# Kernel optimization log

Measured on AMD Instinct MI355X. Metric: run time of the kernel, lower is better.

The kernel has to match this reference:

```python
import jax, jax.numpy as jnp
import numpy as np

B, T, I, H, O, TGT = 64, 512, 64, 512, 64, 96
SCALE = 0.05


def setup_inputs() -> dict:
    key = jax.random.key(0)
    ks = jax.random.split(key, 12)
    rn = lambda k, sh: jax.random.normal(k, sh, jnp.float32) * SCALE
    return {
        "x": jax.random.normal(ks[0], (B, T, I), jnp.float32),
        "W_ih0": rn(ks[1], (4 * H, I)),
        "W_hh0": rn(ks[2], (4 * H, H)),
        "b_ih0": rn(ks[3], (4 * H,)),
        "b_hh0": rn(ks[4], (4 * H,)),
        "W_ih1": rn(ks[5], (4 * H, H)),
        "W_hh1": rn(ks[6], (4 * H, H)),
        "b_ih1": rn(ks[7], (4 * H,)),
        "b_hh1": rn(ks[8], (4 * H,)),
        "W_fc": rn(ks[9], (O, H)),
        "b_fc": rn(ks[10], (O,)),
        "target_len": TGT,
    }


def _cell(x_t, h, c, Wi, Wh, b):
    # PyTorch LSTM gate order: i, f, g, o
    g = x_t @ Wi.T + h @ Wh.T + b  # [B, 4H]
    i, f, gg, o = jnp.split(g, 4, axis=-1)
    c_new = jax.nn.sigmoid(f) * c + jax.nn.sigmoid(i) * jnp.tanh(gg)
    h_new = jax.nn.sigmoid(o) * jnp.tanh(c_new)
    return h_new, c_new


def _run_layer(seq_tbf, Wi, Wh, b):
    # seq_tbf: [T, B, F]; returns hidden sequence [T, B, H] and final (h, c)
    nb = seq_tbf.shape[1]
    hdim = Wh.shape[1]
    init = (jnp.zeros((nb, hdim), seq_tbf.dtype), jnp.zeros((nb, hdim), seq_tbf.dtype))

    def step(carry, x_t):
        h, c = _cell(x_t, carry[0], carry[1], Wi, Wh, b)
        return (h, c), h

    (h, c), hs = jax.lax.scan(step, init, seq_tbf)
    return hs, h, c


def reference(x, W_ih0, W_hh0, b_ih0, b_hh0, W_ih1, W_hh1, b_ih1, b_hh1, W_fc, b_fc, target_len):
    # Dropout is inactive (eval-mode reference).
    b0 = b_ih0 + b_hh0
    b1 = b_ih1 + b_hh1

    # --- encoder pass over full context ---
    seq = jnp.transpose(x, (1, 0, 2))                 # [T, B, I]
    hs0, h0, c0 = _run_layer(seq, W_ih0, W_hh0, b0)   # layer 0
    _, h1, c1 = _run_layer(hs0, W_ih1, W_hh1, b1)     # layer 1

    x_in = x[:, -1, :]  # [B, I]

    def dec_step(carry, _):
        h0, c0, h1, c1, xi = carry
        h0, c0 = _cell(xi, h0, c0, W_ih0, W_hh0, b0)
        h1, c1 = _cell(h0, h1, c1, W_ih1, W_hh1, b1)
        y = h1 @ W_fc.T + b_fc  # [B, O], fed back as next input
        return (h0, c0, h1, c1, y), y

    _, ys = jax.lax.scan(dec_step, (h0, c0, h1, c1, x_in), None, length=target_len)
    return jnp.transpose(ys, (1, 0, 2))  # [B, target_len, O]
```

## Files before the change

### kernel.cpp

```cpp
#include <hip/hip_runtime.h>
#include <stdint.h>


#define NWG 256
#define NTH 256

constexpr int Tt = 512, TGT = 96;

typedef __attribute__((ext_vector_type(8))) short bf16x8;
typedef __attribute__((ext_vector_type(4))) float f32x4;
typedef unsigned long long u64;

__device__ __forceinline__ unsigned short f2bf(float f) {
  union { float f; unsigned u; } v; v.f = f;
  return (unsigned short)((v.u + 0x7fffu + ((v.u >> 16) & 1u)) >> 16);
}
__device__ __forceinline__ float bf2f(unsigned short h) {
  union { unsigned u; float f; } v; v.u = ((unsigned)h) << 16; return v.f;
}
__device__ __forceinline__ float sigm(float x) { return 1.f / (1.f + __expf(-x)); }
__device__ __forceinline__ float tanh_(float x) { return 1.f - 2.f / (__expf(2.f * x) + 1.f); }

__device__ __forceinline__ unsigned ald32a(const unsigned* p) {
  return __hip_atomic_load(p, __ATOMIC_RELAXED, __HIP_MEMORY_SCOPE_AGENT);
}
__device__ __forceinline__ void ast32a(unsigned* p, unsigned v) {
  __hip_atomic_store(p, v, __ATOMIC_RELAXED, __HIP_MEMORY_SCOPE_AGENT);
}
__device__ __forceinline__ u64 ald64a(const u64* p) {
  return __hip_atomic_load(p, __ATOMIC_RELAXED, __HIP_MEMORY_SCOPE_AGENT);
}
__device__ __forceinline__ void ast64a(u64* p, u64 v) {
  __hip_atomic_store(p, v, __ATOMIC_RELAXED, __HIP_MEMORY_SCOPE_AGENT);
}

struct SMem {
  unsigned short wB[2][4][16][64][8];
  u64 a0[16 * 68];
  u64 a1[16 * 68];
  unsigned short wfc2[1024];
  float gpart[4][272];
  float fcp[256];
  float b0s[64], b1s[64], b0d[64], bfc2[2];
};

__device__ __forceinline__ int amap(int idx) {
  int b = idx >> 7, k8 = idx & 127;
  return (k8 >> 3) * 68 + b * 8 + (k8 & 7);
}

__device__ __forceinline__ void stage1(u64* dst, const u64* src, int tid) {
  u64 v0 = ald64a(src + tid),       v1 = ald64a(src + tid + 256);
  u64 v2 = ald64a(src + tid + 512), v3 = ald64a(src + tid + 768);
  dst[amap(tid)] = v0; dst[amap(tid + 256)] = v1;
  dst[amap(tid + 512)] = v2; dst[amap(tid + 768)] = v3;
}
__device__ __forceinline__ void stage2(u64* d0, const u64* s0, u64* d1, const u64* s1, int tid) {
  u64 v0 = ald64a(s0 + tid),       v1 = ald64a(s0 + tid + 256);
  u64 v2 = ald64a(s0 + tid + 512), v3 = ald64a(s0 + tid + 768);
  u64 v4 = ald64a(s1 + tid),       v5 = ald64a(s1 + tid + 256);
  u64 v6 = ald64a(s1 + tid + 512), v7 = ald64a(s1 + tid + 768);
  d0[amap(tid)] = v0; d0[amap(tid + 256)] = v1;
  d0[amap(tid + 512)] = v2; d0[amap(tid + 768)] = v3;
  d1[amap(tid)] = v4; d1[amap(tid + 256)] = v5;
  d1[amap(tid + 512)] = v6; d1[amap(tid + 768)] = v7;
}

__device__ __forceinline__ void gbar(unsigned* slots, int g, int w, unsigned tgt) {
  __syncthreads();
  if (threadIdx.x == 0) ast32a(slots + g * 32 + w, tgt);
  if (threadIdx.x < 64) {
    const unsigned* sp = slots + g * 32 + (threadIdx.x & 31);
    while (true) {
      unsigned v = ald32a(sp);
      if (__all((int)(v >= tgt))) break;
      __builtin_amdgcn_s_sleep(1);
    }
  }
  __syncthreads();
}

#define MFMA(a, b, c) __builtin_amdgcn_mfma_f32_16x16x32_bf16(a, b, c, 0, 0, 0)

__global__ __launch_bounds__(NTH, 1) void lstm_kernel(
    const float* __restrict__ x,
    const float* __restrict__ Wih0, const float* __restrict__ Whh0,
    const float* __restrict__ bih0, const float* __restrict__ bhh0,
    const float* __restrict__ Wih1, const float* __restrict__ Whh1,
    const float* __restrict__ bih1, const float* __restrict__ bhh1,
    const float* __restrict__ Wfc, const float* __restrict__ bfc,
    u64* h0q, u64* h1q, unsigned* slots, float* __restrict__ out)
{
  __shared__ SMem sm;
  const int g = blockIdx.x & 7;
  const int wgw = blockIdx.x >> 3;
  const int tid = threadIdx.x;

  for (int e = tid; e < 8192; e += NTH) {
    int m = e >> 12, w4 = (e >> 10) & 3, kc = (e >> 6) & 15, l = e & 63;
    int colx = l & 15, qx = l >> 4;
    size_t row = (size_t)((colx & 3) * 512 + wgw * 16 + w4 * 4 + (colx >> 2));
    const float* src = (m ? Wih1 : Whh0) + row * 512 + kc * 32 + qx * 8;
    unsigned short* dst = &sm.wB[m][w4][kc][l][0];
    float4 u = *(const float4*)src, v = *(const float4*)(src + 4);
    dst[0] = f2bf(u.x); dst[1] = f2bf(u.y); dst[2] = f2bf(u.z); dst[3] = f2bf(u.w);
    dst[4] = f2bf(v.x); dst[5] = f2bf(v.y); dst[6] = f2bf(v.z); dst[7] = f2bf(v.w);
  }
  for (int e = tid; e < 1024; e += NTH)
    sm.wfc2[e] = f2bf(Wfc[(size_t)(wgw * 2 + (e >> 9)) * 512 + (e & 511)]);
  if (tid < 64) {
    int jj = tid >> 2, g4 = tid & 3;
    int grow = g4 * 512 + wgw * 16 + jj;
    float s0 = bih0[grow] + bhh0[grow];
    sm.b0s[tid] = s0;
    sm.b1s[tid] = bih1[grow] + bhh1[grow];
    float ex = 0.f;
    for (int i = 0; i < 64; ++i) ex += Wih0[(size_t)grow * 64 + i] * bfc[i];
    sm.b0d[tid] = s0 + ex;
  }
  if (tid < 2) sm.bfc2[tid] = bfc[wgw * 2 + tid];

  const int wave = tid >> 6, lane = tid & 63;
  const int col = lane & 15, quad = lane >> 4;
  const int koff = quad * 8;
  const size_t rowg = (size_t)((col & 3) * 512 + wgw * 16 + wave * 4 + (col >> 2));

  bf16x8 whh1f[16];
#pragma unroll
  for (int kc = 0; kc < 16; ++kc) {
    const float* p = Whh1 + rowg * 512 + kc * 32 + koff;
    float4 u = *(const float4*)p, v = *(const float4*)(p + 4);
    bf16x8 r;
    r[0] = (short)f2bf(u.x); r[1] = (short)f2bf(u.y); r[2] = (short)f2bf(u.z); r[3] = (short)f2bf(u.w);
    r[4] = (short)f2bf(v.x); r[5] = (short)f2bf(v.y); r[6] = (short)f2bf(v.z); r[7] = (short)f2bf(v.w);
    whh1f[kc] = r;
  }
  bf16x8 wih0f[2];
#pragma unroll
  for (int kc = 0; kc < 2; ++kc) {
    const float* p = Wih0 + rowg * 64 + kc * 32 + koff;
    float4 u = *(const float4*)p, v = *(const float4*)(p + 4);
    bf16x8 r;
    r[0] = (short)f2bf(u.x); r[1] = (short)f2bf(u.y); r[2] = (short)f2bf(u.z); r[3] = (short)f2bf(u.w);
    r[4] = (short)f2bf(v.x); r[5] = (short)f2bf(v.y); r[6] = (short)f2bf(v.z); r[7] = (short)f2bf(v.w);
    wih0f[kc] = r;
  }
  bf16x8 wcombf[16];
  {
    float wc[16][8];
#pragma unroll
    for (int kc = 0; kc < 16; ++kc)
#pragma unroll
      for (int j = 0; j < 8; ++j) wc[kc][j] = 0.f;
    for (int i = 0; i < 64; ++i) {
      float wi = Wih0[rowg * 64 + i];
      const float* fr = Wfc + (size_t)i * 512 + koff;
#pragma unroll
      for (int kc = 0; kc < 16; ++kc) {
        float4 u = *(const float4*)(fr + kc * 32);
        float4 v = *(const float4*)(fr + kc * 32 + 4);
        wc[kc][0] += wi * u.x; wc[kc][1] += wi * u.y;
        wc[kc][2] += wi * u.z; wc[kc][3] += wi * u.w;
        wc[kc][4] += wi * v.x; wc[kc][5] += wi * v.y;
        wc[kc][6] += wi * v.z; wc[kc][7] += wi * v.w;
      }
    }
#pragma unroll
    for (int kc = 0; kc < 16; ++kc) {
      bf16x8 r;
#pragma unroll
      for (int j = 0; j < 8; ++j) r[j] = (short)f2bf(wc[kc][j]);
      wcombf[kc] = r;
    }
  }
  __syncthreads();

  const float b0c = sm.b0s[wave * 16 + col];
  const float b1c = sm.b1s[wave * 16 + col];
  const float b0dc = sm.b0d[wave * 16 + col];
  const unsigned short* pw0 = &sm.wB[0][wave][0][lane][0];
  const unsigned short* pw1 = &sm.wB[1][wave][0][lane][0];
  const u64* afrag0 = sm.a0 + (col & 7) * 8 + quad * 2;
  const u64* afrag1 = sm.a1 + (col & 7) * 8 + quad * 2;
  unsigned ph = 0;
  float c0 = 0.f, c1 = 0.f;
  const size_t xstride = (size_t)Tt * 64;

  auto loadx = [&](const float* p) -> bf16x8 {
    float4 u = *(const float4*)p, v = *(const float4*)(p + 4);
    bf16x8 r;
    r[0] = (short)f2bf(u.x); r[1] = (short)f2bf(u.y); r[2] = (short)f2bf(u.z); r[3] = (short)f2bf(u.w);
    r[4] = (short)f2bf(v.x); r[5] = (short)f2bf(v.y); r[6] = (short)f2bf(v.z); r[7] = (short)f2bf(v.w);
    return r;
  };

  auto actstore = [&](f32x4 v, float& cst, u64* hdst) {
    float* gp = sm.gpart[wave];
#pragma unroll
    for (int r = 0; r < 4; ++r) gp[(quad * 4 + r) * 17 + col] = v[r];
    unsigned hbits = 0;
    int b = lane >> 2, j = lane & 3;
    if (lane < 32) {
      const float* ro = gp + b * 17 + j * 4;
      float iv = sigm(ro[0]), fv = sigm(ro[1]), gv = tanh_(ro[2]), ov = sigm(ro[3]);
      float c = fv * cst + iv * gv; cst = c;
      hbits = f2bf(ov * tanh_(c));
    }
    unsigned h1b = __shfl(hbits, (lane + 1) & 63);
    unsigned h2b = __shfl(hbits, (lane + 2) & 63);
    unsigned h3b = __shfl(hbits, (lane + 3) & 63);
    if (lane < 32 && j == 0) {
      u64 pk = (u64)hbits | ((u64)h1b << 16) | ((u64)h2b << 32) | ((u64)h3b << 48);
      ast64a(hdst + b * 128 + wgw * 4 + wave, pk);
    }
  };

  auto fcpart = [&](const u64* asrc) {
    int ks = tid >> 4, b = (tid >> 1) & 7, cc = tid & 1;
    const unsigned short* hr = (const unsigned short*)(asrc + ks * 68 + b * 8);
    const unsigned short* wp = sm.wfc2 + cc * 512 + ks * 32;
    float s = 0.f;
#pragma unroll
    for (int k2 = 0; k2 < 4; ++k2) {
      bf16x8 hv = *(const bf16x8*)(hr + k2 * 8);
      bf16x8 wv = *(const bf16x8*)(wp + k2 * 8);
#pragma unroll
      for (int q2 = 0; q2 < 8; ++q2) s += bf2f((unsigned short)hv[q2]) * bf2f((unsigned short)wv[q2]);
    }
    sm.fcp[tid] = s;
  };
  auto fcout = [&](int d) {
    if (tid < 16) {
      float sv = sm.bfc2[tid & 1];
#pragma unroll
      for (int k = 0; k < 16; ++k) sv += sm.fcp[k * 16 + tid];
      int bb = tid >> 1, cc = tid & 1;
      out[(size_t)(g * 8 + bb) * (TGT * 64) + d * 64 + (wgw * 2 + cc)] = sv;
    }
  };

  for (int t = 0; t <= Tt; ++t) {
    const u64* h0prev = h0q + ((t + 1) & 1) * 8192 + g * 1024;
    u64* h0cur = h0q + (t & 1) * 8192 + g * 1024;
    const u64* h1prev = h1q + (t & 1) * 8192 + g * 1024;
    u64* h1cur = h1q + ((t + 1) & 1) * 8192 + g * 1024;

    bf16x8 xa0, xa1;
    if (t < Tt) {
      const float* xb = x + (size_t)(g * 8 + (col & 7)) * xstride + (size_t)t * 64 + koff;
      xa0 = loadx(xb); xa1 = loadx(xb + 32);
    }
    if (t == 1)      { stage1(sm.a0, h0prev, tid); __syncthreads(); }
    else if (t >= 2) { stage2(sm.a0, h0prev, sm.a1, h1prev, tid); __syncthreads(); }

    if (t < Tt) {
      f32x4 za = {b0c, b0c, b0c, b0c}, zb = {0.f, 0.f, 0.f, 0.f};
      za = MFMA(xa0, wih0f[0], za);
      zb = MFMA(xa1, wih0f[1], zb);
      if (t >= 1) {
        f32x4 ya = {b1c, b1c, b1c, b1c}, yb = {0.f, 0.f, 0.f, 0.f};
#pragma unroll
        for (int kc = 0; kc < 16; ++kc) {
          bf16x8 a = *(const bf16x8*)(afrag0 + kc * 68);
          bf16x8 w0 = *(const bf16x8*)(pw0 + kc * 512);
          bf16x8 w1 = *(const bf16x8*)(pw1 + kc * 512);
          if (kc & 1) { zb = MFMA(a, w0, zb); yb = MFMA(a, w1, yb); }
          else        { za = MFMA(a, w0, za); ya = MFMA(a, w1, ya); }
        }
        if (t >= 2) {
#pragma unroll
          for (int kc = 0; kc < 16; ++kc) {
            bf16x8 a = *(const bf16x8*)(afrag1 + kc * 68);
            if (kc & 1) yb = MFMA(a, whh1f[kc], yb);
            else        ya = MFMA(a, whh1f[kc], ya);
          }
        }
        actstore(za + zb, c0, h0cur);
        actstore(ya + yb, c1, h1cur);
      } else {
        actstore(za + zb, c0, h0cur);
      }
    } else {
      f32x4 ya = {b1c, b1c, b1c, b1c}, yb = {0.f, 0.f, 0.f, 0.f};
#pragma unroll
      for (int kc = 0; kc < 16; ++kc) {
        bf16x8 a = *(const bf16x8*)(afrag0 + kc * 68);
        bf16x8 w1 = *(const bf16x8*)(pw1 + kc * 512);
        if (kc & 1) yb = MFMA(a, w1, yb);
        else        ya = MFMA(a, w1, ya);
      }
#pragma unroll
      for (int kc = 0; kc < 16; ++kc) {
        bf16x8 a = *(const bf16x8*)(afrag1 + kc * 68);
        if (kc & 1) yb = MFMA(a, whh1f[kc], yb);
        else        ya = MFMA(a, whh1f[kc], ya);
      }
      actstore(ya + yb, c1, h1cur);
    }
    gbar(slots, g, wgw, ++ph);
  }

  {
    stage2(sm.a0, h0q + 8192 + g * 1024, sm.a1, h1q + 8192 + g * 1024, tid);
    __syncthreads();
    const float* xb = x + (size_t)(g * 8 + (col & 7)) * xstride + (size_t)(Tt - 1) * 64 + koff;
    bf16x8 xa0 = loadx(xb), xa1 = loadx(xb + 32);
    f32x4 za = {b0c, b0c, b0c, b0c}, zb = {0.f, 0.f, 0.f, 0.f};
    za = MFMA(xa0, wih0f[0], za);
    zb = MFMA(xa1, wih0f[1], zb);
#pragma unroll
    for (int kc = 0; kc < 16; ++kc) {
      bf16x8 a = *(const bf16x8*)(afrag0 + kc * 68);
      bf16x8 w0 = *(const bf16x8*)(pw0 + kc * 512);
      if (kc & 1) zb = MFMA(a, w0, zb);
      else        za = MFMA(a, w0, za);
    }
    actstore(za + zb, c0, h0q + g * 1024);
  }
  gbar(slots, g, wgw, ++ph);
  {
    stage1(sm.a0, h0q + g * 1024, tid);
    __syncthreads();
    f32x4 ya = {b1c, b1c, b1c, b1c}, yb = {0.f, 0.f, 0.f, 0.f};
#pragma unroll
    for (int kc = 0; kc < 16; ++kc) {
      bf16x8 a = *(const bf16x8*)(afrag0 + kc * 68);
      bf16x8 w1 = *(const bf16x8*)(pw1 + kc * 512);
      bf16x8 a2 = *(const bf16x8*)(afrag1 + kc * 68);
      if (kc & 1) { yb = MFMA(a, w1, yb); yb = MFMA(a2, whh1f[kc], yb); }
      else        { ya = MFMA(a, w1, ya); ya = MFMA(a2, whh1f[kc], ya); }
    }
    actstore(ya + yb, c1, h1q + g * 1024);
  }
  gbar(slots, g, wgw, ++ph);

  for (int d = 1; d < TGT; ++d) {
    {
      stage2(sm.a0, h0q + ((d + 1) & 1) * 8192 + g * 1024,
             sm.a1, h1q + ((d + 1) & 1) * 8192 + g * 1024, tid);
      __syncthreads();
      fcpart(sm.a1);
      f32x4 za = {b0dc, b0dc, b0dc, b0dc}, zb = {0.f, 0.f, 0.f, 0.f};
#pragma unroll
      for (int kc = 0; kc < 16; ++kc) {
        bf16x8 a = *(const bf16x8*)(afrag0 + kc * 68);
        bf16x8 w0 = *(const bf16x8*)(pw0 + kc * 512);
        bf16x8 a2 = *(const bf16x8*)(afrag1 + kc * 68);
        if (kc & 1) { zb = MFMA(a, w0, zb); zb = MFMA(a2, wcombf[kc], zb); }
        else        { za = MFMA(a, w0, za); za = MFMA(a2, wcombf[kc], za); }
      }
      actstore(za + zb, c0, h0q + (d & 1) * 8192 + g * 1024);
      __syncthreads();
      fcout(d - 1);
    }
    gbar(slots, g, wgw, ++ph);

    {
      stage1(sm.a0, h0q + (d & 1) * 8192 + g * 1024, tid);
      __syncthreads();
      f32x4 ya = {b1c, b1c, b1c, b1c}, yb = {0.f, 0.f, 0.f, 0.f};
#pragma unroll
      for (int kc = 0; kc < 16; ++kc) {
        bf16x8 a = *(const bf16x8*)(afrag0 + kc * 68);
        bf16x8 w1 = *(const bf16x8*)(pw1 + kc * 512);
        bf16x8 a2 = *(const bf16x8*)(afrag1 + kc * 68);
        if (kc & 1) { yb = MFMA(a, w1, yb); yb = MFMA(a2, whh1f[kc], yb); }
        else        { ya = MFMA(a, w1, ya); ya = MFMA(a2, whh1f[kc], ya); }
      }
      actstore(ya + yb, c1, h1q + (d & 1) * 8192 + g * 1024);
    }
    gbar(slots, g, wgw, ++ph);
  }

  {
    stage1(sm.a1, h1q + 8192 + g * 1024, tid);
    __syncthreads();
    fcpart(sm.a1);
    __syncthreads();
    fcout(TGT - 1);
  }
}

extern "C" void kernel_launch(void* const* d_in, const int* in_sizes, int n_in,
                              void* d_out, int out_size, void* d_ws, size_t ws_size,
                              hipStream_t stream) {
  (void)in_sizes; (void)n_in; (void)out_size; (void)ws_size;
  const float* x    = (const float*)d_in[0];
  const float* Wih0 = (const float*)d_in[1];
  const float* Whh0 = (const float*)d_in[2];
  const float* bih0 = (const float*)d_in[3];
  const float* bhh0 = (const float*)d_in[4];
  const float* Wih1 = (const float*)d_in[5];
  const float* Whh1 = (const float*)d_in[6];
  const float* bih1 = (const float*)d_in[7];
  const float* bhh1 = (const float*)d_in[8];
  const float* Wfc  = (const float*)d_in[9];
  const float* bfc  = (const float*)d_in[10];

  char* ws = (char*)d_ws;
  unsigned* slots = (unsigned*)ws;
  u64* h0q = (u64*)(ws + 2048);
  u64* h1q = (u64*)(ws + 2048 + 131072);

  hipMemsetAsync(slots, 0, 2048, stream);
  hipLaunchKernelGGL(lstm_kernel, dim3(NWG), dim3(NTH), 0, stream,
                     x, Wih0, Whh0, bih0, bhh0, Wih1, Whh1, bih1, bhh1, Wfc, bfc,
                     h0q, h1q, slots, (float*)d_out);
}
```

Baseline: 2.910 ms.

## Replace group barriers with tag-embedded data polling on triple-buffered hidden states

Removes the per-step slot barrier across the workgroups of a batch group. Instead, a 2-bit step tag is embedded in the low mantissa bits of selected bf16 hidden values, and consumers poll the hidden-state buffers until every word carries the expected tag. Hidden buffers become triple-buffered so a fast producer cannot overwrite data a slow consumer still needs. The decode prologue is folded into the main loop. The cost is a small perturbation of some bf16 hidden values and spin polling on data words, with correctness resting on the tag and buffer-rotation logic.

```diff
diff --git a/kernel.cpp b/kernel.cpp
--- a/kernel.cpp
+++ b/kernel.cpp
@@ -18,20 +18,32 @@
 __device__ __forceinline__ float bf2f(unsigned short h) {
   union { unsigned u; float f; } v; v.u = ((unsigned)h) << 16; return v.f;
 }
+__device__ __forceinline__ unsigned short f2bf_tag(float f, unsigned bit) {
+  unsigned short b = f2bf(f);
+  if ((b ^ bit) & 1) {
+    if ((b & 0x7fff) == 0) b = (unsigned short)(b | 1);
+    else {
+      unsigned short ca = (unsigned short)(b - 1), cb = (unsigned short)(b + 1);
+      b = (fabsf(f - bf2f(ca)) <= fabsf(f - bf2f(cb))) ? ca : cb;
+    }
+  }
+  return b;
+}
 __device__ __forceinline__ float sigm(float x) { return 1.f / (1.f + __expf(-x)); }
 __device__ __forceinline__ float tanh_(float x) { return 1.f - 2.f / (__expf(2.f * x) + 1.f); }
 
-__device__ __forceinline__ unsigned ald32a(const unsigned* p) {
-  return __hip_atomic_load(p, __ATOMIC_RELAXED, __HIP_MEMORY_SCOPE_AGENT);
-}
-__device__ __forceinline__ void ast32a(unsigned* p, unsigned v) {
-  __hip_atomic_store(p, v, __ATOMIC_RELAXED, __HIP_MEMORY_SCOPE_AGENT);
-}
 __device__ __forceinline__ u64 ald64a(const u64* p) {
   return __hip_atomic_load(p, __ATOMIC_RELAXED, __HIP_MEMORY_SCOPE_AGENT);
 }
 __device__ __forceinline__ void ast64a(u64* p, u64 v) {
   __hip_atomic_store(p, v, __ATOMIC_RELAXED, __HIP_MEMORY_SCOPE_AGENT);
+}
+__device__ __forceinline__ unsigned tag_of(u64 v) {
+  return ((unsigned)v & 1u) | ((((unsigned)(v >> 32)) & 1u) << 1);
+}
+
+__device__ __forceinline__ void wgbar() {
+  asm volatile("s_waitcnt lgkmcnt(0)\n\ts_barrier" ::: "memory");
 }
 
 struct SMem {
@@ -49,35 +61,40 @@
   return (k8 >> 3) * 68 + b * 8 + (k8 & 7);
 }
 
-__device__ __forceinline__ void stage1(u64* dst, const u64* src, int tid) {
-  u64 v0 = ald64a(src + tid),       v1 = ald64a(src + tid + 256);
-  u64 v2 = ald64a(src + tid + 512), v3 = ald64a(src + tid + 768);
+__device__ __forceinline__ u64 polllead(const u64* p, unsigned tg) {
+  u64 v = ald64a(p);
+  while (tag_of(v) != tg) { __builtin_amdgcn_s_sleep(2); v = ald64a(p); }
+  return v;
+}
+__device__ __forceinline__ u64 pollsib(const u64* p, unsigned tg, u64 v) {
+  while (tag_of(v) != tg) { __builtin_amdgcn_s_sleep(1); v = ald64a(p); }
+  return v;
+}
+
+__device__ __forceinline__ void pollstage1(u64* dst, const u64* src, unsigned tg, int tid) {
+  const u64* p = src + tid;
+  u64 v0 = polllead(p, tg);
+  u64 v1 = ald64a(p + 256), v2 = ald64a(p + 512), v3 = ald64a(p + 768);
+  v1 = pollsib(p + 256, tg, v1);
+  v2 = pollsib(p + 512, tg, v2);
+  v3 = pollsib(p + 768, tg, v3);
   dst[amap(tid)] = v0; dst[amap(tid + 256)] = v1;
   dst[amap(tid + 512)] = v2; dst[amap(tid + 768)] = v3;
 }
-__device__ __forceinline__ void stage2(u64* d0, const u64* s0, u64* d1, const u64* s1, int tid) {
-  u64 v0 = ald64a(s0 + tid),       v1 = ald64a(s0 + tid + 256);
-  u64 v2 = ald64a(s0 + tid + 512), v3 = ald64a(s0 + tid + 768);
-  u64 v4 = ald64a(s1 + tid),       v5 = ald64a(s1 + tid + 256);
-  u64 v6 = ald64a(s1 + tid + 512), v7 = ald64a(s1 + tid + 768);
-  d0[amap(tid)] = v0; d0[amap(tid + 256)] = v1;
-  d0[amap(tid + 512)] = v2; d0[amap(tid + 768)] = v3;
-  d1[amap(tid)] = v4; d1[amap(tid + 256)] = v5;
-  d1[amap(tid + 512)] = v6; d1[amap(tid + 768)] = v7;
-}
-
-__device__ __forceinline__ void gbar(unsigned* slots, int g, int w, unsigned tgt) {
-  __syncthreads();
-  if (threadIdx.x == 0) ast32a(slots + g * 32 + w, tgt);
-  if (threadIdx.x < 64) {
-    const unsigned* sp = slots + g * 32 + (threadIdx.x & 31);
-    while (true) {
-      unsigned v = ald32a(sp);
-      if (__all((int)(v >= tgt))) break;
-      __builtin_amdgcn_s_sleep(1);
-    }
-  }
-  __syncthreads();
+__device__ __forceinline__ void pollstage2(u64* d0, const u64* s0, unsigned tg0,
+                                           u64* d1, const u64* s1, unsigned tg1, int tid) {
+  const u64 *p0 = s0 + tid, *p1 = s1 + tid;
+  u64 a = ald64a(p0), b = ald64a(p1);
+  a = pollsib(p0, tg0, a);
+  b = pollsib(p1, tg1, b);
+  u64 a1 = ald64a(p0 + 256), a2 = ald64a(p0 + 512), a3 = ald64a(p0 + 768);
+  u64 b1 = ald64a(p1 + 256), b2 = ald64a(p1 + 512), b3 = ald64a(p1 + 768);
+  a1 = pollsib(p0 + 256, tg0, a1); a2 = pollsib(p0 + 512, tg0, a2); a3 = pollsib(p0 + 768, tg0, a3);
+  b1 = pollsib(p1 + 256, tg1, b1); b2 = pollsib(p1 + 512, tg1, b2); b3 = pollsib(p1 + 768, tg1, b3);
+  d0[amap(tid)] = a;  d0[amap(tid + 256)] = a1;
+  d0[amap(tid + 512)] = a2; d0[amap(tid + 768)] = a3;
+  d1[amap(tid)] = b;  d1[amap(tid + 256)] = b1;
+  d1[amap(tid + 512)] = b2; d1[amap(tid + 768)] = b3;
 }
 
 #define MFMA(a, b, c) __builtin_amdgcn_mfma_f32_16x16x32_bf16(a, b, c, 0, 0, 0)
@@ -89,7 +106,7 @@
     const float* __restrict__ Wih1, const float* __restrict__ Whh1,
     const float* __restrict__ bih1, const float* __restrict__ bhh1,
     const float* __restrict__ Wfc, const float* __restrict__ bfc,
-    u64* h0q, u64* h1q, unsigned* slots, float* __restrict__ out)
+    u64* h0q, u64* h1q, float* __restrict__ out)
 {
   __shared__ SMem sm;
   const int g = blockIdx.x & 7;
@@ -182,9 +199,9 @@
   const unsigned short* pw1 = &sm.wB[1][wave][0][lane][0];
   const u64* afrag0 = sm.a0 + (col & 7) * 8 + quad * 2;
   const u64* afrag1 = sm.a1 + (col & 7) * 8 + quad * 2;
-  unsigned ph = 0;
   float c0 = 0.f, c1 = 0.f;
   const size_t xstride = (size_t)Tt * 64;
+  const int gbase = g * 1024;
 
   auto loadx = [&](const float* p) -> bf16x8 {
     float4 u = *(const float4*)p, v = *(const float4*)(p + 4);
@@ -194,7 +211,7 @@
     return r;
   };
 
-  auto actstore = [&](f32x4 v, float& cst, u64* hdst) {
+  auto actstore = [&](f32x4 v, float& cst, u64* hdst, unsigned tag) {
     float* gp = sm.gpart[wave];
 #pragma unroll
     for (int r = 0; r < 4; ++r) gp[(quad * 4 + r) * 17 + col] = v[r];
@@ -204,7 +221,10 @@
       const float* ro = gp + b * 17 + j * 4;
       float iv = sigm(ro[0]), fv = sigm(ro[1]), gv = tanh_(ro[2]), ov = sigm(ro[3]);
       float c = fv * cst + iv * gv; cst = c;
-      hbits = f2bf(ov * tanh_(c));
+      float hval = ov * tanh_(c);
+      if (j == 0)      hbits = f2bf_tag(hval, tag & 1);
+      else if (j == 2) hbits = f2bf_tag(hval, (tag >> 1) & 1);
+      else             hbits = f2bf(hval);
     }
     unsigned h1b = __shfl(hbits, (lane + 1) & 63);
     unsigned h2b = __shfl(hbits, (lane + 2) & 63);
@@ -240,18 +260,25 @@
   };
 
   for (int t = 0; t <= Tt; ++t) {
-    const u64* h0prev = h0q + ((t + 1) & 1) * 8192 + g * 1024;
-    u64* h0cur = h0q + (t & 1) * 8192 + g * 1024;
-    const u64* h1prev = h1q + (t & 1) * 8192 + g * 1024;
-    u64* h1cur = h1q + ((t + 1) & 1) * 8192 + g * 1024;
-
     bf16x8 xa0, xa1;
     if (t < Tt) {
       const float* xb = x + (size_t)(g * 8 + (col & 7)) * xstride + (size_t)t * 64 + koff;
       xa0 = loadx(xb); xa1 = loadx(xb + 32);
     }
-    if (t == 1)      { stage1(sm.a0, h0prev, tid); __syncthreads(); }
-    else if (t >= 2) { stage2(sm.a0, h0prev, sm.a1, h1prev, tid); __syncthreads(); }
+    if (t == 1) {
+      wgbar();
+      pollstage1(sm.a0, h0q + 0 * 8192 + gbase, 1u, tid);
+      wgbar();
+    } else if (t >= 2) {
+      wgbar();
+      pollstage2(sm.a0, h0q + ((t - 1) % 3) * 8192 + gbase, (unsigned)(t & 3),
+                 sm.a1, h1q + ((t - 2) % 3) * 8192 + gbase, (unsigned)((t - 1) & 3), tid);
+      wgbar();
+    }
+
+    u64* h0cur = h0q + (t % 3) * 8192 + gbase;
+    u64* h1cur = h1q + ((t - 1 + 3) % 3) * 8192 + gbase;
+    unsigned tg0 = (unsigned)((t + 1) & 3), tg1 = (unsigned)(t & 3);
 
     if (t < Tt) {
       f32x4 za = {b0c, b0c, b0c, b0c}, zb = {0.f, 0.f, 0.f, 0.f};
@@ -275,10 +302,10 @@
             else        ya = MFMA(a, whh1f[kc], ya);
           }
         }
-        actstore(za + zb, c0, h0cur);
-        actstore(ya + yb, c1, h1cur);
+        actstore(za + zb, c0, h0cur, tg0);
+        actstore(ya + yb, c1, h1cur, tg1);
       } else {
-        actstore(za + zb, c0, h0cur);
+        actstore(za + zb, c0, h0cur, tg0);
       }
     } else {
       f32x4 ya = {b1c, b1c, b1c, b1c}, yb = {0.f, 0.f, 0.f, 0.f};
@@ -295,69 +322,53 @@
         if (kc & 1) yb = MFMA(a, whh1f[kc], yb);
         else        ya = MFMA(a, whh1f[kc], ya);
       }
-      actstore(ya + yb, c1, h1cur);
-    }
-    gbar(slots, g, wgw, ++ph);
-  }
-
-  {
-    stage2(sm.a0, h0q + 8192 + g * 1024, sm.a1, h1q + 8192 + g * 1024, tid);
-    __syncthreads();
-    const float* xb = x + (size_t)(g * 8 + (col & 7)) * xstride + (size_t)(Tt - 1) * 64 + koff;
-    bf16x8 xa0 = loadx(xb), xa1 = loadx(xb + 32);
-    f32x4 za = {b0c, b0c, b0c, b0c}, zb = {0.f, 0.f, 0.f, 0.f};
-    za = MFMA(xa0, wih0f[0], za);
-    zb = MFMA(xa1, wih0f[1], zb);
-#pragma unroll
-    for (int kc = 0; kc < 16; ++kc) {
-      bf16x8 a = *(const bf16x8*)(afrag0 + kc * 68);
-      bf16x8 w0 = *(const bf16x8*)(pw0 + kc * 512);
-      if (kc & 1) zb = MFMA(a, w0, zb);
-      else        za = MFMA(a, w0, za);
-    }
-    actstore(za + zb, c0, h0q + g * 1024);
-  }
-  gbar(slots, g, wgw, ++ph);
-  {
-    stage1(sm.a0, h0q + g * 1024, tid);
-    __syncthreads();
-    f32x4 ya = {b1c, b1c, b1c, b1c}, yb = {0.f, 0.f, 0.f, 0.f};
-#pragma unroll
-    for (int kc = 0; kc < 16; ++kc) {
-      bf16x8 a = *(const bf16x8*)(afrag0 + kc * 68);
-      bf16x8 w1 = *(const bf16x8*)(pw1 + kc * 512);
-      bf16x8 a2 = *(const bf16x8*)(afrag1 + kc * 68);
-      if (kc & 1) { yb = MFMA(a, w1, yb); yb = MFMA(a2, whh1f[kc], yb); }
-      else        { ya = MFMA(a, w1, ya); ya = MFMA(a2, whh1f[kc], ya); }
-    }
-    actstore(ya + yb, c1, h1q + g * 1024);
-  }
-  gbar(slots, g, wgw, ++ph);
-
-  for (int d = 1; d < TGT; ++d) {
+      actstore(ya + yb, c1, h1cur, tg1);
+    }
+  }
+
+  for (int d = 0; d < TGT; ++d) {
     {
-      stage2(sm.a0, h0q + ((d + 1) & 1) * 8192 + g * 1024,
-             sm.a1, h1q + ((d + 1) & 1) * 8192 + g * 1024, tid);
-      __syncthreads();
-      fcpart(sm.a1);
-      f32x4 za = {b0dc, b0dc, b0dc, b0dc}, zb = {0.f, 0.f, 0.f, 0.f};
-#pragma unroll
-      for (int kc = 0; kc < 16; ++kc) {
-        bf16x8 a = *(const bf16x8*)(afrag0 + kc * 68);
-        bf16x8 w0 = *(const bf16x8*)(pw0 + kc * 512);
-        bf16x8 a2 = *(const bf16x8*)(afrag1 + kc * 68);
-        if (kc & 1) { zb = MFMA(a, w0, zb); zb = MFMA(a2, wcombf[kc], zb); }
-        else        { za = MFMA(a, w0, za); za = MFMA(a2, wcombf[kc], za); }
-      }
-      actstore(za + zb, c0, h0q + (d & 1) * 8192 + g * 1024);
-      __syncthreads();
-      fcout(d - 1);
-    }
-    gbar(slots, g, wgw, ++ph);
+      bf16x8 xa0, xa1;
+      if (d == 0) {
+        const float* xb = x + (size_t)(g * 8 + (col & 7)) * xstride + (size_t)(Tt - 1) * 64 + koff;
+        xa0 = loadx(xb); xa1 = loadx(xb + 32);
+      }
+      wgbar();
+      pollstage2(sm.a0, h0q + ((1 + d) % 3) * 8192 + gbase, (unsigned)(d & 3),
+                 sm.a1, h1q + ((1 + d) % 3) * 8192 + gbase, (unsigned)(d & 3), tid);
+      wgbar();
+      if (d) fcpart(sm.a1);
+      f32x4 za, zb = {0.f, 0.f, 0.f, 0.f};
+      if (d == 0) {
+        za = (f32x4){b0c, b0c, b0c, b0c};
+        za = MFMA(xa0, wih0f[0], za);
+        zb = MFMA(xa1, wih0f[1], zb);
+#pragma unroll
+        for (int kc = 0; kc < 16; ++kc) {
+          bf16x8 a = *(const bf16x8*)(afrag0 + kc * 68);
+          bf16x8 w0 = *(const bf16x8*)(pw0 + kc * 512);
+          if (kc & 1) zb = MFMA(a, w0, zb);
+          else        za = MFMA(a, w0, za);
+        }
+      } else {
+        za = (f32x4){b0dc, b0dc, b0dc, b0dc};
+#pragma unroll
+        for (int kc = 0; kc < 16; ++kc) {
+          bf16x8 a = *(const bf16x8*)(afrag0 + kc * 68);
+          bf16x8 w0 = *(const bf16x8*)(pw0 + kc * 512);
+          bf16x8 a2 = *(const bf16x8*)(afrag1 + kc * 68);
+          if (kc & 1) { zb = MFMA(a, w0, zb); zb = MFMA(a2, wcombf[kc], zb); }
+          else        { za = MFMA(a, w0, za); za = MFMA(a2, wcombf[kc], za); }
+        }
+      }
+      actstore(za + zb, c0, h0q + ((2 + d) % 3) * 8192 + gbase, (unsigned)((d + 1) & 3));
+      if (d) { wgbar(); fcout(d - 1); }
+    }
 
     {
-      stage1(sm.a0, h0q + (d & 1) * 8192 + g * 1024, tid);
-      __syncthreads();
+      wgbar();
+      pollstage1(sm.a0, h0q + ((2 + d) % 3) * 8192 + gbase, (unsigned)((d + 1) & 3), tid);
+      wgbar();
       f32x4 ya = {b1c, b1c, b1c, b1c}, yb = {0.f, 0.f, 0.f, 0.f};
 #pragma unroll
       for (int kc = 0; kc < 16; ++kc) {
@@ -367,16 +378,16 @@
         if (kc & 1) { yb = MFMA(a, w1, yb); yb = MFMA(a2, whh1f[kc], yb); }
         else        { ya = MFMA(a, w1, ya); ya = MFMA(a2, whh1f[kc], ya); }
       }
-      actstore(ya + yb, c1, h1q + (d & 1) * 8192 + g * 1024);
-    }
-    gbar(slots, g, wgw, ++ph);
+      actstore(ya + yb, c1, h1q + ((2 + d) % 3) * 8192 + gbase, (unsigned)((d + 1) & 3));
+    }
   }
 
   {
-    stage1(sm.a1, h1q + 8192 + g * 1024, tid);
-    __syncthreads();
+    wgbar();
+    pollstage1(sm.a1, h1q + 1 * 8192 + gbase, 0u, tid);
+    wgbar();
     fcpart(sm.a1);
-    __syncthreads();
+    wgbar();
     fcout(TGT - 1);
   }
 }
@@ -398,12 +409,11 @@
   const float* bfc  = (const float*)d_in[10];
 
   char* ws = (char*)d_ws;
-  unsigned* slots = (unsigned*)ws;
-  u64* h0q = (u64*)(ws + 2048);
-  u64* h1q = (u64*)(ws + 2048 + 131072);
-
-  hipMemsetAsync(slots, 0, 2048, stream);
+  u64* h0q = (u64*)ws;
+  u64* h1q = (u64*)(ws + 196608);
+
+  hipMemsetAsync(ws, 0xAA, 393216, stream);
   hipLaunchKernelGGL(lstm_kernel, dim3(NWG), dim3(NTH), 0, stream,
                      x, Wih0, Whh0, bih0, bhh0, Wih1, Whh1, bih1, bhh1, Wfc, bfc,
-                     h0q, h1q, slots, (float*)d_out);
-}
+                     h0q, h1q, (float*)d_out);
+}
```

Result: slower. 3.215 ms (+10.5%).
